# Kernel optimization log

Hardware: AMD Instinct MI355X
Metric: run time of the kernel (lower is better)

## Reference

```python
import jax, jax.numpy as jnp
import numpy as np

H = 64          # hidden_channels
N = 65536       # nodes
E = 524288      # edges
G = 256         # graphs in the batch
OUT = 128       # out_channels
NF = 9          # atom feature columns (OGB AtomEncoder)
V = 128         # embedding vocab per feature column
MAX_ITER = 10   # Anderson solver iterations (fixed for jit)
AND_M = 5       # Anderson history depth
LAM = 1e-4      # Anderson Tikhonov regularizer
EPS = 1e-5      # BatchNorm eps


def setup_inputs() -> dict:
    key = jax.random.key(0)
    ks = jax.random.split(key, 16)
    s = 1.0 / np.sqrt(H)
    inp = {}
    # forward args
    inp["data_x"] = jax.random.randint(ks[0], (N, NF), 0, 119)
    inp["edge_index"] = jax.random.randint(ks[1], (2, E), 0, N)
    # small positive weights -> contractive fixed-point map
    inp["edge_weight"] = jax.random.uniform(ks[2], (E,), jnp.float32) * 0.1
    inp["batch"] = jnp.sort(jax.random.randint(ks[3], (N,), 0, G))
    # AtomEncoder: one embedding table per feature column
    inp["emb"] = jax.random.normal(ks[4], (NF, V, H), jnp.float32) * 0.1
    # enc: Linear-GELU-Linear
    inp["W1"] = jax.random.normal(ks[5], (H, H), jnp.float32) * s
    inp["b1"] = jnp.zeros((H,), jnp.float32)
    inp["W2"] = jax.random.normal(ks[6], (H, H), jnp.float32) * s
    inp["b2"] = jnp.zeros((H,), jnp.float32)
    # CayleyLinear: skew generator M and bias
    inp["M"] = jax.random.normal(ks[7], (H, H), jnp.float32) * s
    inp["cb"] = jnp.zeros((H,), jnp.float32)
    # BatchNorm affine params
    inp["bn_gamma"] = jnp.ones((H,), jnp.float32)
    inp["bn_beta"] = jnp.zeros((H,), jnp.float32)
    # dec: Linear-GELU-Linear
    inp["W3"] = jax.random.normal(ks[8], (H, H), jnp.float32) * s
    inp["b3"] = jnp.zeros((H,), jnp.float32)
    inp["W4"] = jax.random.normal(ks[9], (H, OUT), jnp.float32) * s
    inp["b4"] = jnp.zeros((OUT,), jnp.float32)
    return inp


def _anderson(f, z0, max_iter=MAX_ITER, m=AND_M, lam=LAM):
    # Anderson acceleration on the flattened iterate; fixed iteration count.
    shape = z0.shape
    dt = z0.dtype
    flat = lambda z: z.reshape(-1)
    x0 = flat(z0)
    f0 = flat(f(z0))
    X = [x0, f0]
    Fh = [f0, flat(f(f0.reshape(shape)))]
    for k in range(2, max_iter):
        n = min(k, m)
        Xn = jnp.stack(X[-n:])          # [n, d]
        Fn = jnp.stack(Fh[-n:])         # [n, d]
        Gm = Fn - Xn                    # residuals
        Hm = Gm @ Gm.T + lam * jnp.eye(n, dtype=dt)
        alpha = jnp.linalg.solve(Hm, jnp.ones((n,), dt))
        alpha = alpha / alpha.sum()
        xnew = alpha @ Fn               # beta (mixing) = 1
        X.append(xnew)
        Fh.append(flat(f(xnew.reshape(shape))))
    return Fh[-1].reshape(shape)


def reference(data_x, edge_index, edge_weight, batch,
              emb, W1, b1, W2, b2, M, cb, bn_gamma, bn_beta, W3, b3, W4, b4):
    # --- AtomEncoder: sum of per-column embeddings ---
    cols = jnp.arange(NF)[None, :]
    h = emb[cols, data_x, :].sum(axis=1)            # [N, H]
    h = jax.nn.relu(h)
    # --- enc MLP (dropout=0 -> identity) ---
    h = jax.nn.gelu(h @ W1 + b1, approximate=False) @ W2 + b2
    x_inj = h.T                                      # [H, N]
    # --- CayleyLinear: orthogonal W = (I+S)^{-1}(I-S), S skew ---
    S = 0.5 * (M - M.T)
    I = jnp.eye(H, dtype=h.dtype)
    Wc = jnp.linalg.solve(I + S, I - S)              # [H, H]
    src, dst = edge_index[0], edge_index[1]

    def lin(z):                                      # z: [H, N]
        msg = z[:, src] * edge_weight[None, :]       # [H, E] sparse gather
        agg = jax.ops.segment_sum(msg.T, dst, num_segments=N).T  # z @ A
        return Wc @ agg + cb[:, None]

    fmap = lambda z: jax.nn.relu(lin(z) + x_inj)
    zstar = _anderson(fmap, jnp.zeros((H, N), h.dtype))
    x = zstar.T                                      # [N, H]
    # --- BatchNorm1d (training-mode batch stats) ---
    mu = x.mean(axis=0)
    var = x.var(axis=0)
    x = bn_gamma * (x - mu) * jax.lax.rsqrt(var + EPS) + bn_beta
    x = jax.nn.relu(x)
    # --- global_mean_pool ---
    sums = jax.ops.segment_sum(x, batch, num_segments=G)
    cnt = jax.ops.segment_sum(jnp.ones((N,), x.dtype), batch, num_segments=G)
    x = sums / jnp.maximum(cnt, 1.0)[:, None]        # [G, H]
    # --- dec MLP ---
    out = jax.nn.gelu(x @ W3 + b3, approximate=False) @ W4 + b4
    return out                                       # [G, OUT]
```

## Files before the change

### kernel.cpp

```cpp
#include <hip/hip_runtime.h>
#include <math.h>

#define HH   64
#define NN   65536
#define EE   524288
#define GGG  256
#define OUTC 128
#define NFF  9
#define VV   128
#define DTOT (NN*HH)
#define ENC_BLOCKS (NN/64)
#define HIST_BLOCKS (EE/256)

__device__ __forceinline__ float gelu_exact(float x){
    return 0.5f * x * (1.0f + erff(x * 0.70710678118654752f));
}

__global__ __launch_bounds__(256) void setup_kernel(
    const int* __restrict__ dx, const float* __restrict__ emb,
    const float* __restrict__ W1, const float* __restrict__ b1,
    const float* __restrict__ W2, const float* __restrict__ b2,
    float* __restrict__ xinj,
    const float* __restrict__ M, float* __restrict__ WcT,
    const int* __restrict__ batch, int* __restrict__ gstart,
    const int* __restrict__ ei, int* __restrict__ counts)
{
    __shared__ float smem[12352];
    int b = blockIdx.x;
    int t = threadIdx.x;
    if (b == 0){
        float* aug = smem;
        int c = t & 127;
        int h = t >> 7;
        for (int idx = t; idx < 64*128; idx += 256){
            int i = idx >> 7, j = idx & 127, jj = j & 63;
            float s = 0.5f*(M[i*HH+jj] - M[jj*HH+i]);
            float d = (i==jj) ? 1.f : 0.f;
            aug[i*129 + j] = (j < 64) ? (d + s) : (d - s);
        }
        __syncthreads();
        for (int k=0;k<64;++k){
            float piv    = aug[k*129 + k];
            float rowk_c = aug[k*129 + c];
            float fc[32];
            #pragma unroll
            for (int r=0;r<32;++r) fc[r] = aug[(h*32+r)*129 + k];
            __syncthreads();
            float pinv = 1.f/piv;
            float rowk_s = rowk_c * pinv;
            if (c >= k){
                #pragma unroll
                for (int r=0;r<32;++r){
                    int i = h*32 + r;
                    float nv = (i==k) ? rowk_s : fmaf(-fc[r], rowk_s, aug[i*129+c]);
                    aug[i*129+c] = nv;
                }
            }
            __syncthreads();
        }
        for (int idx=t; idx<64*64; idx+=256){
            int k = idx >> 6, cc = idx & 63;
            WcT[k*HH+cc] = aug[cc*129 + 64 + k];
        }
    } else if (b == 1){
        int g = t;
        int lo = 0, hi = NN;
        while (lo < hi){ int mid = (lo+hi)>>1; if (batch[mid] < g) lo = mid+1; else hi = mid; }
        gstart[g] = lo;
        if (g == 0) gstart[GGG] = NN;
    } else if (b < 2 + ENC_BLOCKS){
        float* A   = smem;
        float* W1s = smem + 4160;
        float* W2s = smem + 8256;
        for (int i=t;i<64*64;i+=256){ W1s[i]=W1[i]; W2s[i]=W2[i]; }
        int lane = t & 63;
        int w = t >> 6;
        int tile0 = (b-2) * 64;
        for (int j=0;j<16;++j){
            int nl = w*16 + j;
            int n = tile0 + nl;
            float hsum = 0.f;
            #pragma unroll
            for (int f=0; f<NFF; ++f){
                int idx = dx[n*NFF+f];
                hsum += emb[(f*VV + idx)*HH + lane];
            }
            A[nl*65 + lane] = fmaxf(hsum, 0.f);
        }
        __syncthreads();
        int tn = t & 15;
        int tc = t >> 4;
        float c4[4][4];
        #pragma unroll
        for (int i=0;i<4;++i){
            #pragma unroll
            for (int j=0;j<4;++j) c4[i][j]=0.f;
        }
        #pragma unroll 4
        for (int k=0;k<64;++k){
            float4 bb = *(const float4*)&W1s[k*64 + tc*4];
            #pragma unroll
            for (int i=0;i<4;++i){
                float a = A[(tn+16*i)*65 + k];
                c4[i][0] = fmaf(a, bb.x, c4[i][0]);
                c4[i][1] = fmaf(a, bb.y, c4[i][1]);
                c4[i][2] = fmaf(a, bb.z, c4[i][2]);
                c4[i][3] = fmaf(a, bb.w, c4[i][3]);
            }
        }
        float4 b1v = *(const float4*)&b1[tc*4];
        float b1a[4] = {b1v.x, b1v.y, b1v.z, b1v.w};
        __syncthreads();
        #pragma unroll
        for (int i=0;i<4;++i){
            #pragma unroll
            for (int j=0;j<4;++j)
                A[(tn+16*i)*65 + tc*4+j] = gelu_exact(c4[i][j] + b1a[j]);
        }
        __syncthreads();
        #pragma unroll
        for (int i=0;i<4;++i){
            #pragma unroll
            for (int j=0;j<4;++j) c4[i][j]=0.f;
        }
        #pragma unroll 4
        for (int k=0;k<64;++k){
            float4 bb = *(const float4*)&W2s[k*64 + tc*4];
            #pragma unroll
            for (int i=0;i<4;++i){
                float a = A[(tn+16*i)*65 + k];
                c4[i][0] = fmaf(a, bb.x, c4[i][0]);
                c4[i][1] = fmaf(a, bb.y, c4[i][1]);
                c4[i][2] = fmaf(a, bb.z, c4[i][2]);
                c4[i][3] = fmaf(a, bb.w, c4[i][3]);
            }
        }
        float4 b2v = *(const float4*)&b2[tc*4];
        #pragma unroll
        for (int i=0;i<4;++i){
            int n = tile0 + tn + 16*i;
            float4 o4;
            o4.x = c4[i][0] + b2v.x;
            o4.y = c4[i][1] + b2v.y;
            o4.z = c4[i][2] + b2v.z;
            o4.w = c4[i][3] + b2v.w;
            *(float4*)&xinj[n*HH + tc*4] = o4;
        }
    } else {
        int e = (b - 2 - ENC_BLOCKS)*256 + t;
        if (e < EE) atomicAdd(&counts[ei[EE + e]], 1);
    }
}

__global__ __launch_bounds__(1024) void scan_kernel(const int* __restrict__ counts, int* __restrict__ row_ptr, int* __restrict__ cursor){
    __shared__ int lds[1024];
    int t = threadIdx.x;
    int base = t*64;
    int s=0;
    for (int i=0;i<64;++i) s += counts[base+i];
    lds[t]=s; __syncthreads();
    if (t==0){ int run=0; for (int i=0;i<1024;++i){ int v=lds[i]; lds[i]=run; run+=v; } }
    __syncthreads();
    int run = lds[t];
    for (int i=0;i<64;++i){ row_ptr[base+i]=run; cursor[base+i]=run; run += counts[base+i]; }
    if (t==1023) row_ptr[NN]=run;
}

__global__ void fill_kernel(const int* __restrict__ ei, const float* __restrict__ ew,
                            int* __restrict__ cursor, int2* __restrict__ s_edge){
    int e = blockIdx.x*blockDim.x + threadIdx.x;
    if (e < EE){
        int dstn = ei[EE+e];
        int pos = atomicAdd(&cursor[dstn], 1);
        s_edge[pos] = make_int2(ei[e], __float_as_int(ew[e]));
    }
}

__global__ __launch_bounds__(256) void feval0_kernel(const float* __restrict__ xinj, const float* __restrict__ cb,
                              float* __restrict__ F0, float* __restrict__ G0, float* __restrict__ gram){
    float ps = 0.f;
    int stride = gridDim.x*blockDim.x;
    for (int i = blockIdx.x*blockDim.x + threadIdx.x; i < DTOT; i += stride){
        float v = fmaxf(cb[i&63] + xinj[i], 0.f);
        F0[i]=v; G0[i]=v; ps += v*v;
    }
    #pragma unroll
    for (int off=32; off>0; off>>=1) ps += __shfl_down(ps, off, 64);
    __shared__ float red[4];
    int lane = threadIdx.x&63, w = threadIdx.x>>6;
    if (lane==0) red[w]=ps;
    __syncthreads();
    if (threadIdx.x==0) atomicAdd(&gram[0], red[0]+red[1]+red[2]+red[3]);
}

template<int NOTH, int FINAL>
__global__ __launch_bounds__(256) void feval_kernel(
    const float* __restrict__ z, const float* __restrict__ xinj,
    const float* __restrict__ WcT, const float* __restrict__ cb,
    const int* __restrict__ row_ptr, const int2* __restrict__ s_edge,
    float* __restrict__ Fo, float* __restrict__ Go,
    const float* __restrict__ Gbase, float* __restrict__ gram, int newSlot, int4 oth,
    float* __restrict__ bn1, float* __restrict__ bn2)
{
    __shared__ float A[32*65];
    int t = threadIdx.x;
    const float* gop[4];
    {
        int o4[4] = {oth.x, oth.y, oth.z, oth.w};
        #pragma unroll
        for (int o=0;o<4;++o) gop[o] = Gbase + (size_t)o4[o]*DTOT;
    }
    int lane = t & 63;
    int w = t >> 6;
    int tile0 = blockIdx.x * 32;
    const float* zl = z + lane;
    for (int j=0;j<8;++j){
        int nl = w*8 + j;
        int n = tile0 + nl;
        int e0 = __builtin_amdgcn_readfirstlane(row_ptr[n]);
        int e1 = __builtin_amdgcn_readfirstlane(row_ptr[n+1]);
        float acc = 0.f;
        int e = e0;
        for (; e + 8 <= e1; e += 8){
            int2 p0 = s_edge[e+0], p1 = s_edge[e+1], p2 = s_edge[e+2], p3 = s_edge[e+3];
            int2 p4 = s_edge[e+4], p5 = s_edge[e+5], p6 = s_edge[e+6], p7 = s_edge[e+7];
            float z0 = zl[p0.x*HH];
            float z1 = zl[p1.x*HH];
            float z2 = zl[p2.x*HH];
            float z3 = zl[p3.x*HH];
            float z4 = zl[p4.x*HH];
            float z5 = zl[p5.x*HH];
            float z6 = zl[p6.x*HH];
            float z7 = zl[p7.x*HH];
            acc = fmaf(__int_as_float(p0.y), z0, acc);
            acc = fmaf(__int_as_float(p1.y), z1, acc);
            acc = fmaf(__int_as_float(p2.y), z2, acc);
            acc = fmaf(__int_as_float(p3.y), z3, acc);
            acc = fmaf(__int_as_float(p4.y), z4, acc);
            acc = fmaf(__int_as_float(p5.y), z5, acc);
            acc = fmaf(__int_as_float(p6.y), z6, acc);
            acc = fmaf(__int_as_float(p7.y), z7, acc);
        }
        for (; e + 4 <= e1; e += 4){
            int2 p0 = s_edge[e+0], p1 = s_edge[e+1], p2 = s_edge[e+2], p3 = s_edge[e+3];
            float z0 = zl[p0.x*HH];
            float z1 = zl[p1.x*HH];
            float z2 = zl[p2.x*HH];
            float z3 = zl[p3.x*HH];
            acc = fmaf(__int_as_float(p0.y), z0, acc);
            acc = fmaf(__int_as_float(p1.y), z1, acc);
            acc = fmaf(__int_as_float(p2.y), z2, acc);
            acc = fmaf(__int_as_float(p3.y), z3, acc);
        }
        for (; e < e1; ++e){
            int2 p = s_edge[e];
            acc = fmaf(__int_as_float(p.y), zl[p.x*HH], acc);
        }
        A[nl*65 + lane] = acc;
    }
    __syncthreads();
    int tn = t & 15;
    int tc = t >> 4;
    float c2[2][4];
    #pragma unroll
    for (int i=0;i<2;++i){
        #pragma unroll
        for (int j=0;j<4;++j) c2[i][j]=0.f;
    }
    #pragma unroll 4
    for (int k=0;k<64;++k){
        float4 b = *(const float4*)&WcT[k*64 + tc*4];
        #pragma unroll
        for (int i=0;i<2;++i){
            float a = A[(tn+16*i)*65 + k];
            c2[i][0] = fmaf(a, b.x, c2[i][0]);
            c2[i][1] = fmaf(a, b.y, c2[i][1]);
            c2[i][2] = fmaf(a, b.z, c2[i][2]);
            c2[i][3] = fmaf(a, b.w, c2[i][3]);
        }
    }
    float4 cbv = *(const float4*)&cb[tc*4];
    float p[NOTH+1];
    #pragma unroll
    for (int i=0;i<NOTH+1;++i) p[i]=0.f;
    float bnA[4] = {0.f,0.f,0.f,0.f};
    float bnB[4] = {0.f,0.f,0.f,0.f};
    #pragma unroll
    for (int i=0;i<2;++i){
        int n = tile0 + tn + 16*i;
        int base = n*HH + tc*4;
        float4 xi = *(const float4*)&xinj[base];
        float4 F4;
        F4.x = fmaxf(c2[i][0] + cbv.x + xi.x, 0.f);
        F4.y = fmaxf(c2[i][1] + cbv.y + xi.y, 0.f);
        F4.z = fmaxf(c2[i][2] + cbv.z + xi.z, 0.f);
        F4.w = fmaxf(c2[i][3] + cbv.w + xi.w, 0.f);
        *(float4*)&Fo[base] = F4;
        if constexpr (FINAL){
            bnA[0]+=F4.x; bnB[0]+=F4.x*F4.x;
            bnA[1]+=F4.y; bnB[1]+=F4.y*F4.y;
            bnA[2]+=F4.z; bnB[2]+=F4.z*F4.z;
            bnA[3]+=F4.w; bnB[3]+=F4.w*F4.w;
        } else {
            float4 z4 = *(const float4*)&z[base];
            float4 G4;
            G4.x = F4.x - z4.x; G4.y = F4.y - z4.y;
            G4.z = F4.z - z4.z; G4.w = F4.w - z4.w;
            *(float4*)&Go[base] = G4;
            p[NOTH] += G4.x*G4.x + G4.y*G4.y + G4.z*G4.z + G4.w*G4.w;
            #pragma unroll
            for (int o=0;o<NOTH;++o){
                float4 g4 = *(const float4*)&gop[o][base];
                p[o] += G4.x*g4.x + G4.y*g4.y + G4.z*g4.z + G4.w*g4.w;
            }
        }
    }
    if constexpr (FINAL){
        #pragma unroll
        for (int j=0;j<4;++j){
            #pragma unroll
            for (int off=8; off>0; off>>=1){
                bnA[j] += __shfl_down(bnA[j], off, 16);
                bnB[j] += __shfl_down(bnB[j], off, 16);
            }
        }
        __shared__ float bnredA[64], bnredB[64];
        if (tn==0){
            #pragma unroll
            for (int j=0;j<4;++j){ bnredA[tc*4+j]=bnA[j]; bnredB[tc*4+j]=bnB[j]; }
        }
        __syncthreads();
        if (t < 64){
            int cp = (blockIdx.x & 7) * HH;
            atomicAdd(&bn1[cp+t], bnredA[t]);
            atomicAdd(&bn2[cp+t], bnredB[t]);
        }
    } else {
        #pragma unroll
        for (int i=0;i<NOTH+1;++i){
            #pragma unroll
            for (int off=32; off>0; off>>=1) p[i] += __shfl_down(p[i], off, 64);
        }
        __shared__ float red[4][5];
        if (lane==0){
            #pragma unroll
            for (int i=0;i<NOTH+1;++i) red[w][i]=p[i];
        }
        __syncthreads();
        if (t < NOTH+1){
            float v = red[0][t]+red[1][t]+red[2][t]+red[3][t];
            int o4[4] = {oth.x, oth.y, oth.z, oth.w};
            int tgt = (t==NOTH) ? newSlot : o4[t];
            atomicAdd(&gram[newSlot*5 + tgt], v);
        }
    }
}

__global__ __launch_bounds__(256) void xnew_kernel(const float* __restrict__ Fbase,
                            const float* __restrict__ gram,
                            int n, int w0, float* __restrict__ xnew){
    int sl[5];
    #pragma unroll
    for (int a=0;a<5;++a) sl[a] = (w0+a)%5;
    float A[5][5]; float rhs[5];
    #pragma unroll
    for (int a=0;a<5;++a){
        #pragma unroll
        for (int b=0;b<5;++b){
            float v;
            if (a<n && b<n){
                int wa = (a>b)?a:b;
                int wb = (a>b)?b:a;
                v = gram[sl[wa]*5 + sl[wb]];
            } else v = (a==b)?1.f:0.f;
            A[a][b] = v;
        }
        if (a<n) A[a][a] += 1e-4f;
        rhs[a] = (a<n)? 1.f : 0.f;
    }
    #pragma unroll
    for (int k=0;k<5;++k){
        float inv = 1.f/A[k][k];
        #pragma unroll
        for (int j=0;j<5;++j) A[k][j] *= inv;
        rhs[k] *= inv;
        #pragma unroll
        for (int i=0;i<5;++i){
            if (i==k) continue;
            float f = A[i][k];
            #pragma unroll
            for (int j=0;j<5;++j) A[i][j] -= f*A[k][j];
            rhs[i] -= f*rhs[k];
        }
    }
    float ssum = rhs[0]+rhs[1]+rhs[2]+rhs[3]+rhs[4];
    float invs = 1.f/ssum;
    float a0=rhs[0]*invs, a1=rhs[1]*invs, a2=rhs[2]*invs, a3=rhs[3]*invs, a4=rhs[4]*invs;

    int i = blockIdx.x*blockDim.x+threadIdx.x;
    if (i >= DTOT/4) return;
    const float4* F0 = (const float4*)(Fbase + (size_t)sl[0]*DTOT);
    const float4* F1 = (const float4*)(Fbase + (size_t)sl[1]*DTOT);
    const float4* F2 = (const float4*)(Fbase + (size_t)sl[2]*DTOT);
    const float4* F3 = (const float4*)(Fbase + (size_t)sl[3]*DTOT);
    const float4* F4 = (const float4*)(Fbase + (size_t)sl[4]*DTOT);
    float4 v = F0[i];
    float4 s = make_float4(a0*v.x, a0*v.y, a0*v.z, a0*v.w);
    v = F1[i]; s.x += a1*v.x; s.y += a1*v.y; s.z += a1*v.z; s.w += a1*v.w;
    if (n>2){ v = F2[i]; s.x += a2*v.x; s.y += a2*v.y; s.z += a2*v.z; s.w += a2*v.w; }
    if (n>3){ v = F3[i]; s.x += a3*v.x; s.y += a3*v.y; s.z += a3*v.z; s.w += a3*v.w; }
    if (n>4){ v = F4[i]; s.x += a4*v.x; s.y += a4*v.y; s.z += a4*v.z; s.w += a4*v.w; }
    ((float4*)xnew)[i] = s;
}

__global__ __launch_bounds__(256) void pool_dec_kernel(
    const float* __restrict__ x, const int* __restrict__ gstart,
    const float* __restrict__ bn1, const float* __restrict__ bn2,
    const float* __restrict__ gamma, const float* __restrict__ beta,
    const float* __restrict__ W3, const float* __restrict__ b3,
    const float* __restrict__ W4, const float* __restrict__ b4,
    float* __restrict__ out)
{
    __shared__ float scs[HH], shs[HH];
    __shared__ float red[4][HH];
    __shared__ float pooled[HH];
    __shared__ float tv[HH];
    int g = blockIdx.x;
    int t = threadIdx.x;
    int lane = t & 63, w = t >> 6;
    if (t < HH){
        float a=0.f, b=0.f;
        #pragma unroll
        for (int c=0;c<8;++c){ a += bn1[c*HH+t]; b += bn2[c*HH+t]; }
        float mu  = a*(1.f/NN);
        float var = b*(1.f/NN) - mu*mu;
        float sc = gamma[t]*rsqrtf(var+1e-5f);
        scs[t]=sc; shs[t]=beta[t]-mu*sc;
    }
    __syncthreads();
    int n0 = gstart[g], n1 = gstart[g+1];
    float sc = scs[lane], sh = shs[lane];
    float acc = 0.f;
    for (int n = n0 + w; n < n1; n += 4)
        acc += fmaxf(x[n*HH+lane]*sc + sh, 0.f);
    red[w][lane] = acc;
    __syncthreads();
    if (t < HH){
        float s = red[0][t]+red[1][t]+red[2][t]+red[3][t];
        pooled[t] = s / fmaxf((float)(n1-n0), 1.f);
    }
    __syncthreads();
    if (t < HH){
        float a = b3[t];
        for (int k=0;k<HH;++k) a += pooled[k]*W3[k*HH+t];
        tv[t] = gelu_exact(a);
    }
    __syncthreads();
    if (t < OUTC){
        float o = b4[t];
        for (int c=0;c<HH;++c) o += tv[c]*W4[c*OUTC + t];
        out[g*OUTC + t] = o;
    }
}

static inline void launch_feval(int nOth, int fin, const float* z, const float* xinj, const float* WcT,
                                const float* cb, const int* row_ptr, const int2* s_edge,
                                float* Fo, float* Go, const float* Gbase, float* gram,
                                int newSlot, int4 oth, float* bn1, float* bn2, hipStream_t stream)
{
    if (fin){
        feval_kernel<0,1><<<NN/32,256,0,stream>>>(z,xinj,WcT,cb,row_ptr,s_edge,Fo,Go,Gbase,gram,newSlot,oth,bn1,bn2);
        return;
    }
    switch (nOth){
    case 1: feval_kernel<1,0><<<NN/32,256,0,stream>>>(z,xinj,WcT,cb,row_ptr,s_edge,Fo,Go,Gbase,gram,newSlot,oth,bn1,bn2); break;
    case 2: feval_kernel<2,0><<<NN/32,256,0,stream>>>(z,xinj,WcT,cb,row_ptr,s_edge,Fo,Go,Gbase,gram,newSlot,oth,bn1,bn2); break;
    case 3: feval_kernel<3,0><<<NN/32,256,0,stream>>>(z,xinj,WcT,cb,row_ptr,s_edge,Fo,Go,Gbase,gram,newSlot,oth,bn1,bn2); break;
    default: feval_kernel<4,0><<<NN/32,256,0,stream>>>(z,xinj,WcT,cb,row_ptr,s_edge,Fo,Go,Gbase,gram,newSlot,oth,bn1,bn2); break;
    }
}

extern "C" void kernel_launch(void* const* d_in, const int* in_sizes, int n_in,
                              void* d_out, int out_size, void* d_ws, size_t ws_size,
                              hipStream_t stream)
{
    const int*   dx    = (const int*)d_in[0];
    const int*   ei    = (const int*)d_in[1];
    const float* ew    = (const float*)d_in[2];
    const int*   batch = (const int*)d_in[3];
    const float* emb   = (const float*)d_in[4];
    const float* W1    = (const float*)d_in[5];
    const float* b1    = (const float*)d_in[6];
    const float* W2    = (const float*)d_in[7];
    const float* b2    = (const float*)d_in[8];
    const float* M     = (const float*)d_in[9];
    const float* cb    = (const float*)d_in[10];
    const float* bng   = (const float*)d_in[11];
    const float* bnb   = (const float*)d_in[12];
    const float* W3    = (const float*)d_in[13];
    const float* b3    = (const float*)d_in[14];
    const float* W4    = (const float*)d_in[15];
    const float* b4    = (const float*)d_in[16];
    float* out = (float*)d_out;

    char* wsbase = (char*)d_ws;
    size_t off = 0;
    auto alloc = [&](size_t bytes)->char*{
        char* p = wsbase + off;
        off += (bytes + 255) / 256 * 256;
        return p;
    };
    float* xinj  = (float*)alloc((size_t)DTOT*4);
    float* Fring = (float*)alloc(5*(size_t)DTOT*4);
    float* Gring = (float*)alloc(5*(size_t)DTOT*4);
    float* xbuf  = (float*)alloc((size_t)DTOT*4);
    float* WcT   = (float*)alloc(HH*HH*4);
    float* gram  = (float*)alloc(25*4);
    float* bnbuf = (float*)alloc(2*8*HH*4);
    int*  gstart = (int*)alloc((size_t)(GGG+1)*4);
    int*  counts = (int*)alloc((size_t)NN*4);
    int*  row_ptr= (int*)alloc((size_t)(NN+1)*4);
    int*  cursor = (int*)alloc((size_t)NN*4);
    int2* s_edge = (int2*)alloc((size_t)EE*8);
    float* bn1 = bnbuf;
    float* bn2 = bnbuf + 8*HH;
    (void)ws_size; (void)in_sizes; (void)n_in; (void)out_size;

    hipMemsetAsync(counts, 0, (size_t)NN*4, stream);
    setup_kernel<<<2 + ENC_BLOCKS + HIST_BLOCKS, 256, 0, stream>>>(
        dx, emb, W1,b1,W2,b2, xinj, M, WcT, batch, gstart, ei, counts);
    scan_kernel<<<1,1024,0,stream>>>(counts, row_ptr, cursor);
    fill_kernel<<<EE/256,256,0,stream>>>(ei, ew, cursor, s_edge);

    hipMemsetAsync(gram, 0, 25*4, stream);
    hipMemsetAsync(bnbuf, 0, 2*8*HH*4, stream);
    feval0_kernel<<<1024,256,0,stream>>>(xinj, cb, Fring, Gring, gram);
    {
        int4 oth = make_int4(0,0,0,0);
        launch_feval(1, 0, Fring, xinj, WcT, cb, row_ptr, s_edge,
                     Fring+(size_t)DTOT, Gring+(size_t)DTOT, Gring, gram, 1, oth, bn1, bn2, stream);
    }
    for (int k=2;k<10;++k){
        int n  = (k<5)?k:5;
        int w0 = k-n;
        int slot = k%5;
        xnew_kernel<<<(DTOT/4+255)/256,256,0,stream>>>(Fring, gram, n, w0, xbuf);
        hipMemsetAsync(gram + slot*5, 0, 5*4, stream);
        int nOth = (k<4)?k:4;
        int o4[4] = {0,0,0,0};
        for (int j=1;j<=nOth;++j) o4[j-1] = ((k-j)%5+5)%5;
        int4 oth = make_int4(o4[0],o4[1],o4[2],o4[3]);
        launch_feval(nOth, (k==9)?1:0, xbuf, xinj, WcT, cb, row_ptr, s_edge,
                     Fring+(size_t)slot*DTOT, Gring+(size_t)slot*DTOT, Gring, gram, slot, oth, bn1, bn2, stream);
    }
    float* zstar = Fring + (size_t)(9%5)*DTOT;

    pool_dec_kernel<<<GGG,256,0,stream>>>(zstar, gstart, bn1, bn2, bng, bnb, W3,b3,W4,b4, out);
}
```

Baseline: 997.2 us.

## Balance per-tile edge work across waves with LDS atomics and shrink setup LDS

The SpMM gather now splits all edges of a 32-node tile evenly across the four waves, instead of giving each wave a fixed 8 destination rows. Partial products are accumulated into shared memory with float atomics, using the local destination row packed into the upper bits of the edge record. The Cayley solve is rewritten as an in-place 64x64 Gauss-Jordan inverse, with Wc recovered as 2*inv(I+S)-I. The encoder MLP reads W1 and W2 from global memory instead of staging them in shared memory, which reduces shared memory use. Risks: LDS atomic contention and a changed summation order, and packing the source index into 16 bits only works because N is exactly 65536.

```diff
diff --git a/kernel.cpp b/kernel.cpp
--- a/kernel.cpp
+++ b/kernel.cpp
@@ -25,42 +25,41 @@
     const int* __restrict__ batch, int* __restrict__ gstart,
     const int* __restrict__ ei, int* __restrict__ counts)
 {
-    __shared__ float smem[12352];
+    __shared__ float smem[64*65];
     int b = blockIdx.x;
     int t = threadIdx.x;
     if (b == 0){
-        float* aug = smem;
-        int c = t & 127;
-        int h = t >> 7;
-        for (int idx = t; idx < 64*128; idx += 256){
-            int i = idx >> 7, j = idx & 127, jj = j & 63;
-            float s = 0.5f*(M[i*HH+jj] - M[jj*HH+i]);
-            float d = (i==jj) ? 1.f : 0.f;
-            aug[i*129 + j] = (j < 64) ? (d + s) : (d - s);
+        float* A = smem;
+        int c = t & 63;
+        int h = t >> 6;
+        for (int idx = t; idx < 64*64; idx += 256){
+            int i = idx >> 6, j = idx & 63;
+            float s = 0.5f*(M[i*HH+j] - M[j*HH+i]);
+            A[i*65 + j] = ((i==j)?1.f:0.f) + s;
         }
         __syncthreads();
         for (int k=0;k<64;++k){
-            float piv    = aug[k*129 + k];
-            float rowk_c = aug[k*129 + c];
-            float fc[32];
-            #pragma unroll
-            for (int r=0;r<32;++r) fc[r] = aug[(h*32+r)*129 + k];
+            float piv    = A[k*65 + k];
+            float rowk_c = A[k*65 + c];
+            float fc[16];
+            #pragma unroll
+            for (int r=0;r<16;++r) fc[r] = A[(h*16+r)*65 + k];
             __syncthreads();
             float pinv = 1.f/piv;
             float rowk_s = rowk_c * pinv;
-            if (c >= k){
-                #pragma unroll
-                for (int r=0;r<32;++r){
-                    int i = h*32 + r;
-                    float nv = (i==k) ? rowk_s : fmaf(-fc[r], rowk_s, aug[i*129+c]);
-                    aug[i*129+c] = nv;
-                }
+            #pragma unroll
+            for (int r=0;r<16;++r){
+                int i = h*16 + r;
+                float nv;
+                if (i == k) nv = (c==k) ? pinv : rowk_s;
+                else        nv = (c==k) ? (-fc[r]*pinv) : fmaf(-fc[r], rowk_s, A[i*65+c]);
+                A[i*65+c] = nv;
             }
             __syncthreads();
         }
         for (int idx=t; idx<64*64; idx+=256){
             int k = idx >> 6, cc = idx & 63;
-            WcT[k*HH+cc] = aug[cc*129 + 64 + k];
+            WcT[k*HH+cc] = 2.f*A[cc*65 + k] - ((k==cc)?1.f:0.f);
         }
     } else if (b == 1){
         int g = t;
@@ -69,10 +68,7 @@
         gstart[g] = lo;
         if (g == 0) gstart[GGG] = NN;
     } else if (b < 2 + ENC_BLOCKS){
-        float* A   = smem;
-        float* W1s = smem + 4160;
-        float* W2s = smem + 8256;
-        for (int i=t;i<64*64;i+=256){ W1s[i]=W1[i]; W2s[i]=W2[i]; }
+        float* A = smem;
         int lane = t & 63;
         int w = t >> 6;
         int tile0 = (b-2) * 64;
@@ -98,7 +94,7 @@
         }
         #pragma unroll 4
         for (int k=0;k<64;++k){
-            float4 bb = *(const float4*)&W1s[k*64 + tc*4];
+            float4 bb = *(const float4*)&W1[k*64 + tc*4];
             #pragma unroll
             for (int i=0;i<4;++i){
                 float a = A[(tn+16*i)*65 + k];
@@ -125,7 +121,7 @@
         }
         #pragma unroll 4
         for (int k=0;k<64;++k){
-            float4 bb = *(const float4*)&W2s[k*64 + tc*4];
+            float4 bb = *(const float4*)&W2[k*64 + tc*4];
             #pragma unroll
             for (int i=0;i<4;++i){
                 float a = A[(tn+16*i)*65 + k];
@@ -172,7 +168,7 @@
     if (e < EE){
         int dstn = ei[EE+e];
         int pos = atomicAdd(&cursor[dstn], 1);
-        s_edge[pos] = make_int2(ei[e], __float_as_int(ew[e]));
+        s_edge[pos] = make_int2((ei[e] & 0xFFFF) | ((dstn & 31) << 16), __float_as_int(ew[e]));
     }
 }
 
@@ -214,49 +210,39 @@
     int w = t >> 6;
     int tile0 = blockIdx.x * 32;
     const float* zl = z + lane;
-    for (int j=0;j<8;++j){
-        int nl = w*8 + j;
-        int n = tile0 + nl;
-        int e0 = __builtin_amdgcn_readfirstlane(row_ptr[n]);
-        int e1 = __builtin_amdgcn_readfirstlane(row_ptr[n+1]);
-        float acc = 0.f;
-        int e = e0;
-        for (; e + 8 <= e1; e += 8){
-            int2 p0 = s_edge[e+0], p1 = s_edge[e+1], p2 = s_edge[e+2], p3 = s_edge[e+3];
-            int2 p4 = s_edge[e+4], p5 = s_edge[e+5], p6 = s_edge[e+6], p7 = s_edge[e+7];
-            float z0 = zl[p0.x*HH];
-            float z1 = zl[p1.x*HH];
-            float z2 = zl[p2.x*HH];
-            float z3 = zl[p3.x*HH];
-            float z4 = zl[p4.x*HH];
-            float z5 = zl[p5.x*HH];
-            float z6 = zl[p6.x*HH];
-            float z7 = zl[p7.x*HH];
-            acc = fmaf(__int_as_float(p0.y), z0, acc);
-            acc = fmaf(__int_as_float(p1.y), z1, acc);
-            acc = fmaf(__int_as_float(p2.y), z2, acc);
-            acc = fmaf(__int_as_float(p3.y), z3, acc);
-            acc = fmaf(__int_as_float(p4.y), z4, acc);
-            acc = fmaf(__int_as_float(p5.y), z5, acc);
-            acc = fmaf(__int_as_float(p6.y), z6, acc);
-            acc = fmaf(__int_as_float(p7.y), z7, acc);
-        }
-        for (; e + 4 <= e1; e += 4){
-            int2 p0 = s_edge[e+0], p1 = s_edge[e+1], p2 = s_edge[e+2], p3 = s_edge[e+3];
-            float z0 = zl[p0.x*HH];
-            float z1 = zl[p1.x*HH];
-            float z2 = zl[p2.x*HH];
-            float z3 = zl[p3.x*HH];
-            acc = fmaf(__int_as_float(p0.y), z0, acc);
-            acc = fmaf(__int_as_float(p1.y), z1, acc);
-            acc = fmaf(__int_as_float(p2.y), z2, acc);
-            acc = fmaf(__int_as_float(p3.y), z3, acc);
-        }
-        for (; e < e1; ++e){
-            int2 p = s_edge[e];
-            acc = fmaf(__int_as_float(p.y), zl[p.x*HH], acc);
-        }
-        A[nl*65 + lane] = acc;
+    for (int i=t; i<32*65; i+=256) A[i] = 0.f;
+    __syncthreads();
+    int eStart = __builtin_amdgcn_readfirstlane(row_ptr[tile0]);
+    int eEnd   = __builtin_amdgcn_readfirstlane(row_ptr[tile0+32]);
+    int total  = eEnd - eStart;
+    int per    = (total + 3) >> 2;
+    int we0 = eStart + w*per;
+    int we1 = we0 + per; if (we1 > eEnd) we1 = eEnd; if (we0 > eEnd) we0 = eEnd;
+    int e = we0;
+    for (; e + 8 <= we1; e += 8){
+        int2 p0 = s_edge[e+0], p1 = s_edge[e+1], p2 = s_edge[e+2], p3 = s_edge[e+3];
+        int2 p4 = s_edge[e+4], p5 = s_edge[e+5], p6 = s_edge[e+6], p7 = s_edge[e+7];
+        float z0 = zl[(p0.x & 0xFFFF)*HH];
+        float z1 = zl[(p1.x & 0xFFFF)*HH];
+        float z2 = zl[(p2.x & 0xFFFF)*HH];
+        float z3 = zl[(p3.x & 0xFFFF)*HH];
+        float z4 = zl[(p4.x & 0xFFFF)*HH];
+        float z5 = zl[(p5.x & 0xFFFF)*HH];
+        float z6 = zl[(p6.x & 0xFFFF)*HH];
+        float z7 = zl[(p7.x & 0xFFFF)*HH];
+        atomicAdd(&A[(p0.x >> 16)*65 + lane], __int_as_float(p0.y)*z0);
+        atomicAdd(&A[(p1.x >> 16)*65 + lane], __int_as_float(p1.y)*z1);
+        atomicAdd(&A[(p2.x >> 16)*65 + lane], __int_as_float(p2.y)*z2);
+        atomicAdd(&A[(p3.x >> 16)*65 + lane], __int_as_float(p3.y)*z3);
+        atomicAdd(&A[(p4.x >> 16)*65 + lane], __int_as_float(p4.y)*z4);
+        atomicAdd(&A[(p5.x >> 16)*65 + lane], __int_as_float(p5.y)*z5);
+        atomicAdd(&A[(p6.x >> 16)*65 + lane], __int_as_float(p6.y)*z6);
+        atomicAdd(&A[(p7.x >> 16)*65 + lane], __int_as_float(p7.y)*z7);
+    }
+    for (; e < we1; ++e){
+        int2 p = s_edge[e];
+        float zv = zl[(p.x & 0xFFFF)*HH];
+        atomicAdd(&A[(p.x >> 16)*65 + lane], __int_as_float(p.y)*zv);
     }
     __syncthreads();
     int tn = t & 15;
```

Result: slower. 2.128 ms (+113.4%).
